# Kernel optimization log

Hardware: AMD Instinct MI355X
Metric: run time of the kernel (lower is better)

Reference implementation:

```python
import jax, jax.numpy as jnp
import numpy as np
import math

B, R, D = 2048, 512, 256
OUT = 1


def setup_inputs() -> dict:
    key = jax.random.key(0)
    k1, k2, k3, k4 = jax.random.split(key, 4)
    x = jax.random.normal(k1, (B, D), dtype=jnp.float32)
    th = jnp.zeros((R, D), dtype=jnp.float32)
    sign_param = jax.random.normal(k2, (R, D), dtype=jnp.float32) * 0.1
    mask_logit = jnp.full((R, D), -2.0, dtype=jnp.float32)
    log_kappa = jnp.asarray(math.log(6.0), dtype=jnp.float32)
    head_w = jax.random.normal(k3, (OUT, R), dtype=jnp.float32) * (1.0 / np.sqrt(R))
    head_b = jnp.zeros((OUT,), dtype=jnp.float32)
    return {"x": x, "th": th, "sign_param": sign_param,
            "mask_logit": mask_logit, "log_kappa": log_kappa,
            "head_w": head_w, "head_b": head_b}


def _corner_product_z(x, th, sign_param, mask_logit, log_kappa):
    # x: (B, D); th/sign_param/mask_logit: (R, D)
    kappa = jnp.exp(log_kappa)
    sgn = jnp.tanh(sign_param)                 # soft sign in (-1, 1), (R, D)
    # one-sided threshold predicate, broadcast to (B, R, D)
    s = jax.nn.sigmoid(kappa * sgn[None, :, :] * (x[:, None, :] - th[None, :, :]))
    m = jax.nn.sigmoid(mask_logit)             # soft feature mask, (R, D)
    gated = 1.0 - m[None, :, :] * (1.0 - s)    # masked predicate; m->0 => 1 (ignored)
    z = jnp.prod(gated, axis=-1)               # product over features -> (B, R)
    return z, s, m


def reference(x, th, sign_param, mask_logit, log_kappa, head_w, head_b):
    z, _, _ = _corner_product_z(x, th, sign_param, mask_logit, log_kappa)
    y = z @ head_w.T + head_b                  # (B, OUT)
    return y[..., 0] if OUT == 1 else y
```

## Files before the change

### kernel.cpp

```cpp
#include <hip/hip_runtime.h>
#include <math.h>

#define B_TOT 2048
#define R_TOT 512
#define D_TOT 256
#define LOG2E 1.4426950408889634f
#define SCALE_C 2.220446049250313e-16f

typedef float vf4 __attribute__((ext_vector_type(4)));
typedef float vf2 __attribute__((ext_vector_type(2)));


__global__ void prep_kernel(const float* __restrict__ th,
                            const float* __restrict__ sp,
                            const float* __restrict__ ml,
                            const float* __restrict__ lk,
                            float* __restrict__ pp) {
    int idx = blockIdx.x * 256 + threadIdx.x;
    if (idx >= R_TOT * D_TOT) return;
    float kmul = -LOG2E * __builtin_amdgcn_exp2f(lk[0] * LOG2E);
    float u  = sp[idx];
    float eu = __builtin_amdgcn_exp2f(2.0f * LOG2E * u);
    float t  = 1.0f - 2.0f * __builtin_amdgcn_rcpf(eu + 1.0f);
    float A  = kmul * t;
    float Bc = -A * th[idx];
    float em = __builtin_amdgcn_exp2f(LOG2E * ml[idx]);
    float m1 = __builtin_amdgcn_rcpf(1.0f + em);
    int d = idx & 255;
    pp[idx]                       = A;
    pp[R_TOT * D_TOT + idx]       = Bc;
    pp[2 * R_TOT * D_TOT + idx]   = m1 * (((d & 7) == 0) ? SCALE_C : 1.0f);
}

static __device__ __forceinline__ float pair_swap(float v) {
    int i = __builtin_amdgcn_mov_dpp(__float_as_int(v), 0xB1, 0xF, 0xF, true);
    return __int_as_float(i);
}

__global__ __launch_bounds__(256, 4) void main_kernel(
        const float* __restrict__ x,
        const float* __restrict__ pp,
        const float* __restrict__ head_w,
        const float* __restrict__ head_b,
        float*       __restrict__ y) {
    __shared__ float rbuf[4][16][36];
    __shared__ float wz[4][16];

    const int tid  = threadIdx.x;
    const int lane = tid & 63;
    const int wave = tid >> 6;
    const int r0   = (blockIdx.x << 2) + wave;
    const int b0   = blockIdx.y << 4;

    const vf4* pA = (const vf4*)pp                         + r0 * 64 + lane;
    const vf4* pB = (const vf4*)(pp + R_TOT * D_TOT)       + r0 * 64 + lane;
    const vf4* pM = (const vf4*)(pp + 2 * R_TOT * D_TOT)   + r0 * 64 + lane;
    vf4 A  = *pA;
    vf4 Bc = *pB;
    vf4 Ms = *pM;
    const float kx = (lane & 1) ? 1.0f : SCALE_C;
    const vf4 K = {kx, 1.0f, 1.0f, 1.0f};

    const vf4* xv = (const vf4*)x + (size_t)b0 * 64 + lane;

    float r8[16];
    #pragma unroll
    for (int b = 0; b < 16; b++) {
        vf4 xb = xv[b * 64];
        vf4 t  = A * xb + Bc;
        vf4 e;
        e.x = __builtin_amdgcn_exp2f(t.x);
        e.y = __builtin_amdgcn_exp2f(t.y);
        e.z = __builtin_amdgcn_exp2f(t.z);
        e.w = __builtin_amdgcn_exp2f(t.w);
        vf4 n  = Ms * e + K;
        vf4 dd = e * K + K;
        vf2 hn = n.lo * n.hi;
        vf2 hd = dd.lo * dd.hi;
        float np = hn.x * hn.y;
        float dp = hd.x * hd.y;
        float np8 = np * pair_swap(np);
        float dp8 = dp * pair_swap(dp);
        r8[b] = np8 * __builtin_amdgcn_rcpf(dp8);
    }

    if (!(lane & 1)) {
        #pragma unroll
        for (int b = 0; b < 16; b++)
            rbuf[wave][b][lane >> 1] = r8[b];
    }
    __syncthreads();

    if (lane < 16) {
        const float* rb = &rbuf[wave][lane][0];
        vf4 a0 = *(const vf4*)(rb)      * *(const vf4*)(rb + 4);
        vf4 a1 = *(const vf4*)(rb + 8)  * *(const vf4*)(rb + 12);
        vf4 a2 = *(const vf4*)(rb + 16) * *(const vf4*)(rb + 20);
        vf4 a3 = *(const vf4*)(rb + 24) * *(const vf4*)(rb + 28);
        vf4 m  = (a0 * a1) * (a2 * a3);
        vf2 h  = m.lo * m.hi;
        float z = h.x * h.y;
        wz[wave][lane] = head_w[r0] * z;
    }
    __syncthreads();

    if (wave == 0 && lane < 16) {
        float s = wz[0][lane] + wz[1][lane] + wz[2][lane] + wz[3][lane];
        if (blockIdx.x == 0) s += head_b[0];
        atomicAdd(&y[b0 + lane], s);
    }
}

extern "C" void kernel_launch(void* const* d_in, const int* in_sizes, int n_in,
                              void* d_out, int out_size, void* d_ws, size_t ws_size,
                              hipStream_t stream) {
    const float* x  = (const float*)d_in[0];
    const float* th = (const float*)d_in[1];
    const float* sp = (const float*)d_in[2];
    const float* ml = (const float*)d_in[3];
    const float* lk = (const float*)d_in[4];
    const float* hw = (const float*)d_in[5];
    const float* hb = (const float*)d_in[6];
    float* y = (float*)d_out;

    float* pp = (float*)d_ws;

    hipMemsetAsync(y, 0, (size_t)out_size * sizeof(float), stream);
    prep_kernel<<<R_TOT, 256, 0, stream>>>(th, sp, ml, lk, pp);
    dim3 grid(R_TOT / 4, B_TOT / 16, 1);
    main_kernel<<<grid, 256, 0, stream>>>(x, pp, hw, hb, y);
}
```

Baseline: 125.2 us.

## Give each lane 8 features and share one reciprocal across two batch rows

Each lane now handles 8 contiguous features for two batch rows at once, so the DPP pair-swap is no longer needed. One reciprocal of the product of both denominators replaces two reciprocals. All lanes now write partial ratios straight to shared memory. Zeroing y moves from a separate memset into the prep kernel, removing one launch. The cost is more registers per lane and a slightly different rounding order in the division.

```diff
diff --git a/kernel.cpp b/kernel.cpp
--- a/kernel.cpp
+++ b/kernel.cpp
@@ -15,8 +15,10 @@
                             const float* __restrict__ sp,
                             const float* __restrict__ ml,
                             const float* __restrict__ lk,
-                            float* __restrict__ pp) {
+                            float* __restrict__ pp,
+                            float* __restrict__ y) {
     int idx = blockIdx.x * 256 + threadIdx.x;
+    if (blockIdx.x < (B_TOT / 256)) y[idx] = 0.0f;
     if (idx >= R_TOT * D_TOT) return;
     float kmul = -LOG2E * __builtin_amdgcn_exp2f(lk[0] * LOG2E);
     float u  = sp[idx];
@@ -32,11 +34,6 @@
     pp[2 * R_TOT * D_TOT + idx]   = m1 * (((d & 7) == 0) ? SCALE_C : 1.0f);
 }
 
-static __device__ __forceinline__ float pair_swap(float v) {
-    int i = __builtin_amdgcn_mov_dpp(__float_as_int(v), 0xB1, 0xF, 0xF, true);
-    return __int_as_float(i);
-}
-
 __global__ __launch_bounds__(256, 4) void main_kernel(
         const float* __restrict__ x,
         const float* __restrict__ pp,
@@ -49,54 +46,90 @@
     const int tid  = threadIdx.x;
     const int lane = tid & 63;
     const int wave = tid >> 6;
+    const int col  = lane & 31;
+    const int p    = lane >> 5;
     const int r0   = (blockIdx.x << 2) + wave;
     const int b0   = blockIdx.y << 4;
 
-    const vf4* pA = (const vf4*)pp                         + r0 * 64 + lane;
-    const vf4* pB = (const vf4*)(pp + R_TOT * D_TOT)       + r0 * 64 + lane;
-    const vf4* pM = (const vf4*)(pp + 2 * R_TOT * D_TOT)   + r0 * 64 + lane;
-    vf4 A  = *pA;
-    vf4 Bc = *pB;
-    vf4 Ms = *pM;
-    const float kx = (lane & 1) ? 1.0f : SCALE_C;
-    const vf4 K = {kx, 1.0f, 1.0f, 1.0f};
+    const float* ppr = pp + r0 * D_TOT + (col << 3);
+    vf4 A0  = *(const vf4*)(ppr);
+    vf4 A1  = *(const vf4*)(ppr + 4);
+    vf4 Bc0 = *(const vf4*)(ppr + R_TOT * D_TOT);
+    vf4 Bc1 = *(const vf4*)(ppr + R_TOT * D_TOT + 4);
+    vf4 M0  = *(const vf4*)(ppr + 2 * R_TOT * D_TOT);
+    vf4 M1  = *(const vf4*)(ppr + 2 * R_TOT * D_TOT + 4);
+    const vf4 Klo = {SCALE_C, 1.0f, 1.0f, 1.0f};
 
-    const vf4* xv = (const vf4*)x + (size_t)b0 * 64 + lane;
+    const float* xb = x + (size_t)(b0 + p) * D_TOT + (col << 3);
 
-    float r8[16];
     #pragma unroll
-    for (int b = 0; b < 16; b++) {
-        vf4 xb = xv[b * 64];
-        vf4 t  = A * xb + Bc;
-        vf4 e;
-        e.x = __builtin_amdgcn_exp2f(t.x);
-        e.y = __builtin_amdgcn_exp2f(t.y);
-        e.z = __builtin_amdgcn_exp2f(t.z);
-        e.w = __builtin_amdgcn_exp2f(t.w);
-        vf4 n  = Ms * e + K;
-        vf4 dd = e * K + K;
-        vf2 hn = n.lo * n.hi;
-        vf2 hd = dd.lo * dd.hi;
-        float np = hn.x * hn.y;
-        float dp = hd.x * hd.y;
-        float np8 = np * pair_swap(np);
-        float dp8 = dp * pair_swap(dp);
-        r8[b] = np8 * __builtin_amdgcn_rcpf(dp8);
+    for (int q = 0; q < 4; q++) {
+        const float* xq = xb + q * (4 * D_TOT);
+        vf4 xa0 = *(const vf4*)(xq);
+        vf4 xa1 = *(const vf4*)(xq + 4);
+        vf4 xc0 = *(const vf4*)(xq + 2 * D_TOT);
+        vf4 xc1 = *(const vf4*)(xq + 2 * D_TOT + 4);
+
+        vf4 ta0 = A0 * xa0 + Bc0;
+        vf4 ta1 = A1 * xa1 + Bc1;
+        vf4 tc0 = A0 * xc0 + Bc0;
+        vf4 tc1 = A1 * xc1 + Bc1;
+
+        vf4 ea0, ea1, ec0, ec1;
+        ea0.x = __builtin_amdgcn_exp2f(ta0.x);
+        ea0.y = __builtin_amdgcn_exp2f(ta0.y);
+        ea0.z = __builtin_amdgcn_exp2f(ta0.z);
+        ea0.w = __builtin_amdgcn_exp2f(ta0.w);
+        ea1.x = __builtin_amdgcn_exp2f(ta1.x);
+        ea1.y = __builtin_amdgcn_exp2f(ta1.y);
+        ea1.z = __builtin_amdgcn_exp2f(ta1.z);
+        ea1.w = __builtin_amdgcn_exp2f(ta1.w);
+        ec0.x = __builtin_amdgcn_exp2f(tc0.x);
+        ec0.y = __builtin_amdgcn_exp2f(tc0.y);
+        ec0.z = __builtin_amdgcn_exp2f(tc0.z);
+        ec0.w = __builtin_amdgcn_exp2f(tc0.w);
+        ec1.x = __builtin_amdgcn_exp2f(tc1.x);
+        ec1.y = __builtin_amdgcn_exp2f(tc1.y);
+        ec1.z = __builtin_amdgcn_exp2f(tc1.z);
+        ec1.w = __builtin_amdgcn_exp2f(tc1.w);
+
+        vf4 na0 = M0 * ea0 + Klo;
+        vf4 na1 = M1 * ea1 + 1.0f;
+        vf4 da0 = ea0 * Klo + Klo;
+        vf4 da1 = ea1 + 1.0f;
+        vf4 nc0 = M0 * ec0 + Klo;
+        vf4 nc1 = M1 * ec1 + 1.0f;
+        vf4 dc0 = ec0 * Klo + Klo;
+        vf4 dc1 = ec1 + 1.0f;
+
+        vf4 qn_a = na0 * na1;
+        vf4 qd_a = da0 * da1;
+        vf4 qn_c = nc0 * nc1;
+        vf4 qd_c = dc0 * dc1;
+        vf2 hn_a = qn_a.lo * qn_a.hi;
+        vf2 hd_a = qd_a.lo * qd_a.hi;
+        vf2 hn_c = qn_c.lo * qn_c.hi;
+        vf2 hd_c = qd_c.lo * qd_c.hi;
+        float npA = hn_a.x * hn_a.y;
+        float dpA = hd_a.x * hd_a.y;
+        float npC = hn_c.x * hn_c.y;
+        float dpC = hd_c.x * hd_c.y;
+
+        float inv = __builtin_amdgcn_rcpf(dpA * dpC);
+        float rA  = npA * (dpC * inv);
+        float rC  = npC * (dpA * inv);
+        rbuf[wave][4 * q + p][col]     = rA;
+        rbuf[wave][4 * q + 2 + p][col] = rC;
     }
 
-    if (!(lane & 1)) {
-        #pragma unroll
-        for (int b = 0; b < 16; b++)
-            rbuf[wave][b][lane >> 1] = r8[b];
-    }
     __syncthreads();
 
     if (lane < 16) {
-        const float* rb = &rbuf[wave][lane][0];
-        vf4 a0 = *(const vf4*)(rb)      * *(const vf4*)(rb + 4);
-        vf4 a1 = *(const vf4*)(rb + 8)  * *(const vf4*)(rb + 12);
-        vf4 a2 = *(const vf4*)(rb + 16) * *(const vf4*)(rb + 20);
-        vf4 a3 = *(const vf4*)(rb + 24) * *(const vf4*)(rb + 28);
+        const float* rb2 = &rbuf[wave][lane][0];
+        vf4 a0 = *(const vf4*)(rb2)      * *(const vf4*)(rb2 + 4);
+        vf4 a1 = *(const vf4*)(rb2 + 8)  * *(const vf4*)(rb2 + 12);
+        vf4 a2 = *(const vf4*)(rb2 + 16) * *(const vf4*)(rb2 + 20);
+        vf4 a3 = *(const vf4*)(rb2 + 24) * *(const vf4*)(rb2 + 28);
         vf4 m  = (a0 * a1) * (a2 * a3);
         vf2 h  = m.lo * m.hi;
         float z = h.x * h.y;
@@ -125,8 +158,7 @@
 
     float* pp = (float*)d_ws;
 
-    hipMemsetAsync(y, 0, (size_t)out_size * sizeof(float), stream);
-    prep_kernel<<<R_TOT, 256, 0, stream>>>(th, sp, ml, lk, pp);
+    prep_kernel<<<R_TOT, 256, 0, stream>>>(th, sp, ml, lk, pp, y);
     dim3 grid(R_TOT / 4, B_TOT / 16, 1);
     main_kernel<<<grid, 256, 0, stream>>>(x, pp, hw, hb, y);
 }
```

After: 117.1 us. 1.07x faster.
